# Kernel optimization log

Hardware: AMD Instinct MI355X
Metric: run time of the kernel (lower is better)

## Reference

```python
import jax, jax.numpy as jnp
import numpy as np

NUM_NODES = 50000
NUM_EDGES = 800000
NUM_GRAPHS = 1024
D_IN = 64
D_PROT = 1280
HID = 256
OUT = 1


def setup_inputs() -> dict:
    key = jax.random.key(0)
    ks = jax.random.split(key, 16)
    s = 0.02
    x = jax.random.normal(ks[0], (NUM_NODES, D_IN), dtype=jnp.float32)
    edge_index = jax.random.randint(ks[1], (2, NUM_EDGES), 0, NUM_NODES, dtype=jnp.int32)
    batch = jnp.sort(jax.random.randint(ks[2], (NUM_NODES,), 0, NUM_GRAPHS, dtype=jnp.int32))
    protein_embedding = jax.random.normal(ks[3], (NUM_GRAPHS, D_PROT), dtype=jnp.float32)
    # SAGEConv params: lin_l (aggregated neighbors, with bias), lin_r (self, no bias)
    Wl = jax.random.normal(ks[4], (D_IN, HID), dtype=jnp.float32) * s
    bl = jnp.zeros((HID,), dtype=jnp.float32)
    Wr = jax.random.normal(ks[5], (D_IN, HID), dtype=jnp.float32) * s
    Wp = jax.random.normal(ks[6], (D_PROT, HID), dtype=jnp.float32) * s
    bp = jnp.zeros((HID,), dtype=jnp.float32)
    Wi = jax.random.normal(ks[7], (2 * HID, HID), dtype=jnp.float32) * s
    bi = jnp.zeros((HID,), dtype=jnp.float32)
    Wo = jax.random.normal(ks[8], (HID, OUT), dtype=jnp.float32) * s
    bo = jnp.zeros((OUT,), dtype=jnp.float32)
    return {"x": x, "protein_embedding": protein_embedding, "Wl": Wl, "bl": bl,
            "Wr": Wr, "Wp": Wp, "bp": bp, "Wi": Wi, "bi": bi, "Wo": Wo, "bo": bo,
            "edge_index": edge_index, "batch": batch}


def _segment_mean(vals, seg_ids, num_segments):
    sums = jax.ops.segment_sum(vals, seg_ids, num_segments=num_segments)
    cnt = jax.ops.segment_sum(jnp.ones((vals.shape[0],), vals.dtype), seg_ids,
                              num_segments=num_segments)
    return sums / jnp.maximum(cnt, 1.0)[:, None]


def reference(x, protein_embedding, Wl, bl, Wr, Wp, bp, Wi, bi, Wo, bo, edge_index, batch):
    src, dst = edge_index[0], edge_index[1]
    # SAGEConv: mean-aggregate neighbor messages at target nodes, then fuse linears
    aggr = _segment_mean(x[src], dst, NUM_NODES)           # [N, D_IN]
    drug_x = jax.nn.relu(aggr @ Wl + bl + x @ Wr)          # [N, HID]
    # global_mean_pool over graphs in the batch
    pooled = _segment_mean(drug_x, batch, NUM_GRAPHS)      # [G, HID]
    protein_x = protein_embedding @ Wp + bp                # [G, HID]
    combined = jnp.concatenate((pooled, protein_x), axis=1)  # [G, 2*HID]
    interaction = jax.nn.relu(combined @ Wi + bi)          # [G, HID]
    return interaction @ Wo + bo                           # [G, OUT]
```

## Files before the change

### kernel.cpp

```cpp
#include <hip/hip_runtime.h>
#include <hip/hip_bf16.h>

#define N_NODES 50000
#define N_EDGES 800000
#define N_GRAPHS 1024
#define D_IN 64
#define D_PROT 1280
#define HID 256
#define N_PAD 50048

#define NB 782
#define BCAP 2048
#define BEPB 4096
#define BBLK 196

typedef __attribute__((ext_vector_type(8))) short short8;
typedef __attribute__((ext_vector_type(4))) float f32x4;
typedef __hip_bfloat16 bf16;

__device__ inline unsigned bf16rne(float f) {
  unsigned u = __float_as_uint(f);
  return (u + 0x7fffu + ((u >> 16) & 1u)) >> 16;
}
__device__ inline void acc_bf2(float4& a, uint2 v) {
  a.x += __uint_as_float(v.x << 16);
  a.y += __uint_as_float(v.x & 0xffff0000u);
  a.z += __uint_as_float(v.y << 16);
  a.w += __uint_as_float(v.y & 0xffff0000u);
}

#define PREP_XC 3125
#define PREP_PE (PREP_XC + 1280)
#define PREP_PL (PREP_PE + 8)
#define PREP_PR (PREP_PL + 8)
#define PREP_WP (PREP_PR + 160)
#define PREP_WI (PREP_WP + 64)

__device__ inline void pack_frag(const float* __restrict__ src, bf16* __restrict__ dst,
                                 int KC, int tid) {
  int lane = tid & 63;
  int chunk = tid >> 6;
  int c = chunk / KC, kc = chunk - c * KC;
  int kbase = kc * 32 + ((lane >> 4) * 8);
  int n = c * 16 + (lane & 15);
#pragma unroll
  for (int j = 0; j < 8; ++j)
    dst[(size_t)tid * 8 + j] = __float2bfloat16(src[(size_t)(kbase + j) * HID + n]);
}

__global__ __launch_bounds__(256) void k_front(
    const float* __restrict__ x, const float* __restrict__ pe,
    const float* __restrict__ Wl, const float* __restrict__ Wr,
    const float* __restrict__ Wp, const float* __restrict__ Wi,
    const int* __restrict__ ei,
    uint2* __restrict__ x2, uint2* __restrict__ pe2,
    bf16* __restrict__ Wl_pk, bf16* __restrict__ Wr_pk,
    bf16* __restrict__ Wp_pk, bf16* __restrict__ Wi_pk,
    int* __restrict__ bcnt, unsigned* __restrict__ bped) {
  __shared__ int hist[NB];
  __shared__ int base[NB];
  const int b = blockIdx.x;
  const int t = threadIdx.x;
  if (b < BBLK) {
    const int e0 = b * BEPB;
    for (int i = t; i < NB; i += 256) hist[i] = 0;
    __syncthreads();
    for (int i = t; i < BEPB; i += 1024) {
      int d[4]; bool v[4];
#pragma unroll
      for (int u = 0; u < 4; ++u) {
        int idx = i + u * 256;
        v[u] = (e0 + idx < N_EDGES);
        d[u] = v[u] ? ei[N_EDGES + e0 + idx] : 0;
      }
#pragma unroll
      for (int u = 0; u < 4; ++u)
        if (v[u]) atomicAdd(&hist[d[u] >> 6], 1);
    }
    __syncthreads();
    for (int i = t; i < NB; i += 256) {
      int c = hist[i];
      base[i] = (c > 0) ? atomicAdd(&bcnt[i], c) : 0;
      hist[i] = 0;
    }
    __syncthreads();
    for (int i = t; i < BEPB; i += 1024) {
      int s[4], d[4]; bool v[4];
#pragma unroll
      for (int u = 0; u < 4; ++u) {
        int idx = i + u * 256;
        v[u] = (e0 + idx < N_EDGES);
        s[u] = v[u] ? ei[e0 + idx] : 0;
        d[u] = v[u] ? ei[N_EDGES + e0 + idx] : 0;
      }
#pragma unroll
      for (int u = 0; u < 4; ++u) {
        if (v[u]) {
          int bk = d[u] >> 6;
          int pos = base[bk] + atomicAdd(&hist[bk], 1);
          if (pos < BCAP)
            bped[(size_t)bk * BCAP + pos] =
                (unsigned)s[u] | ((unsigned)(d[u] & 63) << 16);
        }
      }
    }
    return;
  }
  const int pb = b - BBLK;
  if (pb < PREP_XC) {
    int tid = pb * 256 + t;
    float4 v = ((const float4*)x)[tid];
    x2[tid] = make_uint2(bf16rne(v.x) | (bf16rne(v.y) << 16),
                         bf16rne(v.z) | (bf16rne(v.w) << 16));
  } else if (pb < PREP_PE) {
    int tid = (pb - PREP_XC) * 256 + t;
    float4 v = ((const float4*)pe)[tid];
    pe2[tid] = make_uint2(bf16rne(v.x) | (bf16rne(v.y) << 16),
                          bf16rne(v.z) | (bf16rne(v.w) << 16));
  } else if (pb < PREP_PL) {
    pack_frag(Wl, Wl_pk, 2, (pb - PREP_PE) * 256 + t);
  } else if (pb < PREP_PR) {
    pack_frag(Wr, Wr_pk, 2, (pb - PREP_PL) * 256 + t);
  } else if (pb < PREP_WP) {
    pack_frag(Wp, Wp_pk, 40, (pb - PREP_PR) * 256 + t);
  } else {
    pack_frag(Wi, Wi_pk, 16, (pb - PREP_WP) * 256 + t);
  }
}

__global__ __launch_bounds__(256) void k_mid(
    const uint2* __restrict__ x2, const unsigned* __restrict__ bped,
    const int* __restrict__ bcnt, uint2* __restrict__ a2,
    const bf16* __restrict__ pebf, const bf16* __restrict__ Wp_pk,
    float* __restrict__ prot4) {
  __shared__ unsigned s_raw[BCAP];
  __shared__ unsigned short s_e[BCAP];
  __shared__ int s_off[65];
  __shared__ int s_cur[64];
  const int t = threadIdx.x;
  if (blockIdx.x < NB) {
    const int b = blockIdx.x;
    const int nE = min(bcnt[b], BCAP);
    if (t < 64) s_cur[t] = 0;
    __syncthreads();
    for (int i = t; i < nE; i += 256) {
      unsigned pk = bped[(size_t)b * BCAP + i];
      s_raw[i] = pk;
      atomicAdd(&s_cur[(pk >> 16) & 63], 1);
    }
    __syncthreads();
    if (t < 64) {
      int sc = s_cur[t];
#pragma unroll
      for (int off = 1; off < 64; off <<= 1) {
        int u = __shfl_up(sc, off);
        if (t >= off) sc += u;
      }
      s_off[t + 1] = sc;
      if (t == 0) s_off[0] = 0;
      s_cur[t] = 0;
    }
    __syncthreads();
    for (int i = t; i < nE; i += 256) {
      unsigned pk = s_raw[i];
      int ld = (pk >> 16) & 63;
      int pos = s_off[ld] + atomicAdd(&s_cur[ld], 1);
      s_e[pos] = (unsigned short)(pk & 0xffffu);
    }
    __syncthreads();

    const int w = t >> 6, lane = t & 63;
    const int el = lane >> 4;
    const int fb = lane & 15;
    for (int n = w; n < 64; n += 4) {
      const int beg = s_off[n], end = s_off[n + 1];
      float4 s0 = {0,0,0,0}, s1 = {0,0,0,0}, s2 = {0,0,0,0}, s3 = {0,0,0,0};
      int e = beg;
      for (; e + 16 <= end; e += 16) {
        int i0 = s_e[e + el],     i1 = s_e[e + 4 + el];
        int i2 = s_e[e + 8 + el], i3 = s_e[e + 12 + el];
        uint2 v0 = x2[(size_t)i0 * 16 + fb];
        uint2 v1 = x2[(size_t)i1 * 16 + fb];
        uint2 v2 = x2[(size_t)i2 * 16 + fb];
        uint2 v3 = x2[(size_t)i3 * 16 + fb];
        acc_bf2(s0, v0); acc_bf2(s1, v1); acc_bf2(s2, v2); acc_bf2(s3, v3);
      }
      for (; e + 4 <= end; e += 4)
        acc_bf2(s0, x2[(size_t)s_e[e + el] * 16 + fb]);
      if (e + el < end)
        acc_bf2(s1, x2[(size_t)s_e[e + el] * 16 + fb]);
      float4 tt;
      tt.x = (s0.x + s1.x) + (s2.x + s3.x);
      tt.y = (s0.y + s1.y) + (s2.y + s3.y);
      tt.z = (s0.z + s1.z) + (s2.z + s3.z);
      tt.w = (s0.w + s1.w) + (s2.w + s3.w);
      tt.x += __shfl_xor(tt.x, 32); tt.x += __shfl_xor(tt.x, 16);
      tt.y += __shfl_xor(tt.y, 32); tt.y += __shfl_xor(tt.y, 16);
      tt.z += __shfl_xor(tt.z, 32); tt.z += __shfl_xor(tt.z, 16);
      tt.w += __shfl_xor(tt.w, 32); tt.w += __shfl_xor(tt.w, 16);
      const int node = b * 64 + n;
      if (el == 0 && node < N_NODES) {
        float inv = 1.0f / (float)max(end - beg, 1);
        uint2 o;
        o.x = bf16rne(tt.x * inv) | (bf16rne(tt.y * inv) << 16);
        o.y = bf16rne(tt.z * inv) | (bf16rne(tt.w * inv) << 16);
        a2[(size_t)node * 16 + fb] = o;
      }
    }
    return;
  }
  const int kb = blockIdx.x - NB;
  const int w = t >> 6, lane = t & 63;
  const int ml = lane & 15, q = lane >> 4;
  const int mt = kb >> 2, ks = kb & 3;
  const int g0 = mt * 16, kc0 = ks * 10;
  f32x4 acc[4];
#pragma unroll
  for (int c = 0; c < 4; ++c) acc[c] = (f32x4){0.f, 0.f, 0.f, 0.f};
  for (int kc = kc0; kc < kc0 + 10; ++kc) {
    short8 a = *(const short8*)(pebf + (size_t)(g0 + ml) * D_PROT + kc * 32 + q * 8);
#pragma unroll
    for (int cl = 0; cl < 4; ++cl) {
      short8 bb = *(const short8*)(Wp_pk + ((size_t)((w * 4 + cl) * 40 + kc) * 64 + lane) * 8);
      acc[cl] = __builtin_amdgcn_mfma_f32_16x16x32_bf16(a, bb, acc[cl], 0, 0, 0);
    }
  }
#pragma unroll
  for (int cl = 0; cl < 4; ++cl) {
    const int col = w * 64 + cl * 16 + ml;
#pragma unroll
    for (int i = 0; i < 4; ++i)
      prot4[((size_t)ks * N_GRAPHS + g0 + q * 4 + i) * HID + col] = acc[cl][i];
  }
}

__global__ __launch_bounds__(256) void k_mlp(
    const bf16* __restrict__ aggrbf, const bf16* __restrict__ xbf,
    const bf16* __restrict__ Wl_pk, const bf16* __restrict__ Wr_pk,
    const float* __restrict__ bl, unsigned short* __restrict__ drug) {
  const int t = threadIdx.x, w = t >> 6, lane = t & 63;
  const int ml = lane & 15, q = lane >> 4;
  const int n0 = blockIdx.x * 64;

  f32x4 acc[4][4];
#pragma unroll
  for (int a = 0; a < 4; ++a)
#pragma unroll
    for (int c = 0; c < 4; ++c) acc[a][c] = (f32x4){0.f, 0.f, 0.f, 0.f};

#pragma unroll
  for (int mat = 0; mat < 2; ++mat) {
    const bf16* A = mat ? xbf : aggrbf;
    const bf16* B = mat ? Wr_pk : Wl_pk;
#pragma unroll
    for (int kc = 0; kc < 2; ++kc) {
      short8 af[4], bfr[4];
#pragma unroll
      for (int rt = 0; rt < 4; ++rt)
        af[rt] = *(const short8*)(A + (size_t)(n0 + rt * 16 + ml) * D_IN + kc * 32 + q * 8);
#pragma unroll
      for (int cl = 0; cl < 4; ++cl)
        bfr[cl] = *(const short8*)(B + ((size_t)((w * 4 + cl) * 2 + kc) * 64 + lane) * 8);
#pragma unroll
      for (int rt = 0; rt < 4; ++rt)
#pragma unroll
        for (int cl = 0; cl < 4; ++cl)
          acc[rt][cl] = __builtin_amdgcn_mfma_f32_16x16x32_bf16(af[rt], bfr[cl], acc[rt][cl], 0, 0, 0);
    }
  }

#pragma unroll
  for (int cl = 0; cl < 4; ++cl) {
    const int col = w * 64 + cl * 16 + ml;
    const float bias = bl[col];
#pragma unroll
    for (int rt = 0; rt < 4; ++rt) {
#pragma unroll
      for (int i = 0; i < 4; ++i) {
        const int row = n0 + rt * 16 + q * 4 + i;
        drug[(size_t)row * HID + col] =
            (unsigned short)bf16rne(fmaxf(acc[rt][cl][i] + bias, 0.f));
      }
    }
  }
}

__device__ inline int lb_dev(const int* __restrict__ a, int v) {
  int lo = 0, hi = N_NODES;
  while (lo < hi) { int m = (lo + hi) >> 1; if (a[m] < v) lo = m + 1; else hi = m; }
  return lo;
}

__global__ __launch_bounds__(256) void k_pool(
    const unsigned short* __restrict__ drug, const int* __restrict__ batch,
    const float* __restrict__ prot4, const float* __restrict__ bp,
    unsigned short* __restrict__ comb) {
  const int t = threadIdx.x;
  if (blockIdx.x < N_GRAPHS) {
    const int g = blockIdx.x;
    const int lo = lb_dev(batch, g);
    const int hi = lb_dev(batch, g + 1);
    float s0 = 0.f, s1 = 0.f, s2 = 0.f, s3 = 0.f;
    float s4 = 0.f, s5 = 0.f, s6 = 0.f, s7 = 0.f;
    int r = lo;
    for (; r + 8 <= hi; r += 8) {
      s0 += __uint_as_float((unsigned)drug[(size_t)(r + 0) * HID + t] << 16);
      s1 += __uint_as_float((unsigned)drug[(size_t)(r + 1) * HID + t] << 16);
      s2 += __uint_as_float((unsigned)drug[(size_t)(r + 2) * HID + t] << 16);
      s3 += __uint_as_float((unsigned)drug[(size_t)(r + 3) * HID + t] << 16);
      s4 += __uint_as_float((unsigned)drug[(size_t)(r + 4) * HID + t] << 16);
      s5 += __uint_as_float((unsigned)drug[(size_t)(r + 5) * HID + t] << 16);
      s6 += __uint_as_float((unsigned)drug[(size_t)(r + 6) * HID + t] << 16);
      s7 += __uint_as_float((unsigned)drug[(size_t)(r + 7) * HID + t] << 16);
    }
    for (; r < hi; ++r)
      s0 += __uint_as_float((unsigned)drug[(size_t)r * HID + t] << 16);
    float inv = 1.0f / (float)max(hi - lo, 1);
    float m = (((s0 + s1) + (s2 + s3)) + ((s4 + s5) + (s6 + s7))) * inv;
    comb[(size_t)g * 512 + t] = (unsigned short)bf16rne(m);
    return;
  }
  const int pb = blockIdx.x - N_GRAPHS;
#pragma unroll
  for (int g = 0; g < 4; ++g) {
    const int gg = pb * 4 + g;
    size_t idx = (size_t)gg * HID + t;
    float pr = prot4[idx] + prot4[(size_t)N_GRAPHS * HID + idx]
             + prot4[2 * (size_t)N_GRAPHS * HID + idx]
             + prot4[3 * (size_t)N_GRAPHS * HID + idx];
    comb[(size_t)gg * 512 + HID + t] = (unsigned short)bf16rne(pr + bp[t]);
  }
}

__global__ __launch_bounds__(256) void k_tail(
    const bf16* __restrict__ comb, const bf16* __restrict__ Wi_pk,
    const float* __restrict__ bi, const float* __restrict__ Wo,
    const float* __restrict__ bo, float* __restrict__ out) {
  __shared__ float sRed[16 * 4];
  const int t = threadIdx.x, w = t >> 6, lane = t & 63;
  const int ml = lane & 15, q = lane >> 4;
  const int g0 = blockIdx.x * 16;
  f32x4 acc[4];
#pragma unroll
  for (int c = 0; c < 4; ++c) acc[c] = (f32x4){0.f, 0.f, 0.f, 0.f};
  for (int kc = 0; kc < 16; ++kc) {
    short8 a = *(const short8*)(comb + (size_t)(g0 + ml) * 512 + kc * 32 + q * 8);
#pragma unroll
    for (int cl = 0; cl < 4; ++cl) {
      short8 bb = *(const short8*)(Wi_pk + ((size_t)((w * 4 + cl) * 16 + kc) * 64 + lane) * 8);
      acc[cl] = __builtin_amdgcn_mfma_f32_16x16x32_bf16(a, bb, acc[cl], 0, 0, 0);
    }
  }
  float bic[4], woc[4];
#pragma unroll
  for (int cl = 0; cl < 4; ++cl) {
    const int col = w * 64 + cl * 16 + ml;
    bic[cl] = bi[col];
    woc[cl] = Wo[col];
  }
#pragma unroll
  for (int i = 0; i < 4; ++i) {
    float s = 0.f;
#pragma unroll
    for (int cl = 0; cl < 4; ++cl)
      s += fmaxf(acc[cl][i] + bic[cl], 0.f) * woc[cl];
    s += __shfl_xor(s, 1); s += __shfl_xor(s, 2);
    s += __shfl_xor(s, 4); s += __shfl_xor(s, 8);
    if (ml == 0) sRed[(q * 4 + i) * 4 + w] = s;
  }
  __syncthreads();
  if (t < 16)
    out[g0 + t] = sRed[t * 4 + 0] + sRed[t * 4 + 1] + sRed[t * 4 + 2]
                + sRed[t * 4 + 3] + bo[0];
}

extern "C" void kernel_launch(void* const* d_in, const int* in_sizes, int n_in,
                              void* d_out, int out_size, void* d_ws, size_t ws_size,
                              hipStream_t stream) {
  const float* x     = (const float*)d_in[0];
  const float* pe    = (const float*)d_in[1];
  const float* Wl    = (const float*)d_in[2];
  const float* bl    = (const float*)d_in[3];
  const float* Wr    = (const float*)d_in[4];
  const float* Wp    = (const float*)d_in[5];
  const float* bp    = (const float*)d_in[6];
  const float* Wi    = (const float*)d_in[7];
  const float* bi    = (const float*)d_in[8];
  const float* Wo    = (const float*)d_in[9];
  const float* bo    = (const float*)d_in[10];
  const int*   ei    = (const int*)d_in[11];
  const int*   batch = (const int*)d_in[12];
  float* out = (float*)d_out;

  char* p = (char*)d_ws;
  auto alloc = [&](size_t bytes) {
    char* r = p;
    p += (bytes + 255) & ~(size_t)255;
    return r;
  };
  int*      bcnt  = (int*)alloc(NB * 4);
  size_t zbytes = (size_t)(p - (char*)d_ws);
  unsigned* bped  = (unsigned*)alloc((size_t)NB * BCAP * 4);
  bf16*  xbf    = (bf16*)alloc((size_t)N_PAD * D_IN * 2);
  bf16*  aggrbf = (bf16*)alloc((size_t)N_PAD * D_IN * 2);
  bf16*  pebf   = (bf16*)alloc((size_t)N_GRAPHS * D_PROT * 2);
  bf16*  Wl_pk  = (bf16*)alloc((size_t)D_IN * HID * 2);
  bf16*  Wr_pk  = (bf16*)alloc((size_t)D_IN * HID * 2);
  bf16*  Wp_pk  = (bf16*)alloc((size_t)D_PROT * HID * 2);
  bf16*  Wi_pk  = (bf16*)alloc((size_t)2 * HID * HID * 2);
  float* prot4  = (float*)alloc((size_t)4 * N_GRAPHS * HID * 4);
  unsigned short* drug = (unsigned short*)alloc((size_t)N_PAD * HID * 2);
  unsigned short* comb = (unsigned short*)alloc((size_t)N_GRAPHS * 2 * HID * 2);

  (void)hipMemsetAsync(d_ws, 0, zbytes, stream);

  k_front<<<BBLK + PREP_WI, 256, 0, stream>>>(
      x, pe, Wl, Wr, Wp, Wi, ei,
      (uint2*)xbf, (uint2*)pebf, Wl_pk, Wr_pk, Wp_pk, Wi_pk, bcnt, bped);
  k_mid<<<NB + 256, 256, 0, stream>>>(
      (const uint2*)xbf, bped, bcnt, (uint2*)aggrbf, pebf, Wp_pk, prot4);
  k_mlp<<<N_PAD / 64, 256, 0, stream>>>(aggrbf, xbf, Wl_pk, Wr_pk, bl, drug);
  k_pool<<<N_GRAPHS + 256, 256, 0, stream>>>(drug, batch, prot4, bp, comb);
  k_tail<<<N_GRAPHS / 16, 256, 0, stream>>>((const bf16*)comb, Wi_pk, bi, Wo, bo, out);
}
```

Baseline: 171.1 us.

## Fuse neighbor aggregation with SAGE linear layers and drop split-K protein GEMM

Merges the mean-aggregation kernel and the node MLP kernel so each block keeps its 64 aggregated rows in shared memory and immediately runs the Wl/Wr MFMA GEMM. This removes the aggregated-feature round trip through global memory and one kernel launch. The protein projection now runs as a full-K GEMM in 64 blocks and writes bf16 with bias straight into the combined buffer, which drops the fp32 split-K partials and their reduction in the pool kernel. The trade-off is more shared memory and registers per block in the fused kernel, and fewer, longer protein blocks.

```diff
diff --git a/kernel.cpp b/kernel.cpp
--- a/kernel.cpp
+++ b/kernel.cpp
@@ -13,6 +13,8 @@
 #define BCAP 2048
 #define BEPB 4096
 #define BBLK 196
+
+#define AGG_STRIDE 72
 
 typedef __attribute__((ext_vector_type(8))) short short8;
 typedef __attribute__((ext_vector_type(4))) float f32x4;
@@ -128,16 +130,22 @@
   }
 }
 
-__global__ __launch_bounds__(256) void k_mid(
+__global__ __launch_bounds__(256) void k_fuse(
     const uint2* __restrict__ x2, const unsigned* __restrict__ bped,
-    const int* __restrict__ bcnt, uint2* __restrict__ a2,
+    const int* __restrict__ bcnt, const bf16* __restrict__ xbf,
+    const bf16* __restrict__ Wl_pk, const bf16* __restrict__ Wr_pk,
+    const float* __restrict__ bl,
     const bf16* __restrict__ pebf, const bf16* __restrict__ Wp_pk,
-    float* __restrict__ prot4) {
+    const float* __restrict__ bp,
+    unsigned short* __restrict__ drug, unsigned short* __restrict__ comb) {
   __shared__ unsigned s_raw[BCAP];
   __shared__ unsigned short s_e[BCAP];
   __shared__ int s_off[65];
   __shared__ int s_cur[64];
+  __shared__ unsigned short s_agg[64 * AGG_STRIDE];
   const int t = threadIdx.x;
+  const int w = t >> 6, lane = t & 63;
+  const int ml = lane & 15, q = lane >> 4;
   if (blockIdx.x < NB) {
     const int b = blockIdx.x;
     const int nE = min(bcnt[b], BCAP);
@@ -169,9 +177,8 @@
     }
     __syncthreads();
 
-    const int w = t >> 6, lane = t & 63;
-    const int el = lane >> 4;
-    const int fb = lane & 15;
+    const int el = q;
+    const int fb = ml;
     for (int n = w; n < 64; n += 4) {
       const int beg = s_off[n], end = s_off[n + 1];
       float4 s0 = {0,0,0,0}, s1 = {0,0,0,0}, s2 = {0,0,0,0}, s3 = {0,0,0,0};
@@ -198,26 +205,73 @@
       tt.y += __shfl_xor(tt.y, 32); tt.y += __shfl_xor(tt.y, 16);
       tt.z += __shfl_xor(tt.z, 32); tt.z += __shfl_xor(tt.z, 16);
       tt.w += __shfl_xor(tt.w, 32); tt.w += __shfl_xor(tt.w, 16);
-      const int node = b * 64 + n;
-      if (el == 0 && node < N_NODES) {
+      if (el == 0) {
         float inv = 1.0f / (float)max(end - beg, 1);
         uint2 o;
         o.x = bf16rne(tt.x * inv) | (bf16rne(tt.y * inv) << 16);
         o.y = bf16rne(tt.z * inv) | (bf16rne(tt.w * inv) << 16);
-        a2[(size_t)node * 16 + fb] = o;
+        *(uint2*)(s_agg + n * AGG_STRIDE + fb * 4) = o;
+      }
+    }
+    __syncthreads();
+
+    const int n0 = b * 64;
+    f32x4 acc[4][4];
+#pragma unroll
+    for (int a = 0; a < 4; ++a)
+#pragma unroll
+      for (int c = 0; c < 4; ++c) acc[a][c] = (f32x4){0.f, 0.f, 0.f, 0.f};
+#pragma unroll
+    for (int kc = 0; kc < 2; ++kc) {
+      short8 af[4], bfr[4];
+#pragma unroll
+      for (int rt = 0; rt < 4; ++rt)
+        af[rt] = *(const short8*)(s_agg + (rt * 16 + ml) * AGG_STRIDE + kc * 32 + q * 8);
+#pragma unroll
+      for (int cl = 0; cl < 4; ++cl)
+        bfr[cl] = *(const short8*)(Wl_pk + ((size_t)((w * 4 + cl) * 2 + kc) * 64 + lane) * 8);
+#pragma unroll
+      for (int rt = 0; rt < 4; ++rt)
+#pragma unroll
+        for (int cl = 0; cl < 4; ++cl)
+          acc[rt][cl] = __builtin_amdgcn_mfma_f32_16x16x32_bf16(af[rt], bfr[cl], acc[rt][cl], 0, 0, 0);
+    }
+#pragma unroll
+    for (int kc = 0; kc < 2; ++kc) {
+      short8 af[4], bfr[4];
+#pragma unroll
+      for (int rt = 0; rt < 4; ++rt)
+        af[rt] = *(const short8*)(xbf + (size_t)(n0 + rt * 16 + ml) * D_IN + kc * 32 + q * 8);
+#pragma unroll
+      for (int cl = 0; cl < 4; ++cl)
+        bfr[cl] = *(const short8*)(Wr_pk + ((size_t)((w * 4 + cl) * 2 + kc) * 64 + lane) * 8);
+#pragma unroll
+      for (int rt = 0; rt < 4; ++rt)
+#pragma unroll
+        for (int cl = 0; cl < 4; ++cl)
+          acc[rt][cl] = __builtin_amdgcn_mfma_f32_16x16x32_bf16(af[rt], bfr[cl], acc[rt][cl], 0, 0, 0);
+    }
+#pragma unroll
+    for (int cl = 0; cl < 4; ++cl) {
+      const int col = w * 64 + cl * 16 + ml;
+      const float bias = bl[col];
+#pragma unroll
+      for (int rt = 0; rt < 4; ++rt) {
+#pragma unroll
+        for (int i = 0; i < 4; ++i) {
+          const int row = n0 + rt * 16 + q * 4 + i;
+          drug[(size_t)row * HID + col] =
+              (unsigned short)bf16rne(fmaxf(acc[rt][cl][i] + bias, 0.f));
+        }
       }
     }
     return;
   }
-  const int kb = blockIdx.x - NB;
-  const int w = t >> 6, lane = t & 63;
-  const int ml = lane & 15, q = lane >> 4;
-  const int mt = kb >> 2, ks = kb & 3;
-  const int g0 = mt * 16, kc0 = ks * 10;
+  const int g0 = (blockIdx.x - NB) * 16;
   f32x4 acc[4];
 #pragma unroll
   for (int c = 0; c < 4; ++c) acc[c] = (f32x4){0.f, 0.f, 0.f, 0.f};
-  for (int kc = kc0; kc < kc0 + 10; ++kc) {
+  for (int kc = 0; kc < 40; ++kc) {
     short8 a = *(const short8*)(pebf + (size_t)(g0 + ml) * D_PROT + kc * 32 + q * 8);
 #pragma unroll
     for (int cl = 0; cl < 4; ++cl) {
@@ -228,60 +282,11 @@
 #pragma unroll
   for (int cl = 0; cl < 4; ++cl) {
     const int col = w * 64 + cl * 16 + ml;
+    const float bias = bp[col];
 #pragma unroll
     for (int i = 0; i < 4; ++i)
-      prot4[((size_t)ks * N_GRAPHS + g0 + q * 4 + i) * HID + col] = acc[cl][i];
-  }
-}
-
-__global__ __launch_bounds__(256) void k_mlp(
-    const bf16* __restrict__ aggrbf, const bf16* __restrict__ xbf,
-    const bf16* __restrict__ Wl_pk, const bf16* __restrict__ Wr_pk,
-    const float* __restrict__ bl, unsigned short* __restrict__ drug) {
-  const int t = threadIdx.x, w = t >> 6, lane = t & 63;
-  const int ml = lane & 15, q = lane >> 4;
-  const int n0 = blockIdx.x * 64;
-
-  f32x4 acc[4][4];
-#pragma unroll
-  for (int a = 0; a < 4; ++a)
-#pragma unroll
-    for (int c = 0; c < 4; ++c) acc[a][c] = (f32x4){0.f, 0.f, 0.f, 0.f};
-
-#pragma unroll
-  for (int mat = 0; mat < 2; ++mat) {
-    const bf16* A = mat ? xbf : aggrbf;
-    const bf16* B = mat ? Wr_pk : Wl_pk;
-#pragma unroll
-    for (int kc = 0; kc < 2; ++kc) {
-      short8 af[4], bfr[4];
-#pragma unroll
-      for (int rt = 0; rt < 4; ++rt)
-        af[rt] = *(const short8*)(A + (size_t)(n0 + rt * 16 + ml) * D_IN + kc * 32 + q * 8);
-#pragma unroll
-      for (int cl = 0; cl < 4; ++cl)
-        bfr[cl] = *(const short8*)(B + ((size_t)((w * 4 + cl) * 2 + kc) * 64 + lane) * 8);
-#pragma unroll
-      for (int rt = 0; rt < 4; ++rt)
-#pragma unroll
-        for (int cl = 0; cl < 4; ++cl)
-          acc[rt][cl] = __builtin_amdgcn_mfma_f32_16x16x32_bf16(af[rt], bfr[cl], acc[rt][cl], 0, 0, 0);
-    }
-  }
-
-#pragma unroll
-  for (int cl = 0; cl < 4; ++cl) {
-    const int col = w * 64 + cl * 16 + ml;
-    const float bias = bl[col];
-#pragma unroll
-    for (int rt = 0; rt < 4; ++rt) {
-#pragma unroll
-      for (int i = 0; i < 4; ++i) {
-        const int row = n0 + rt * 16 + q * 4 + i;
-        drug[(size_t)row * HID + col] =
-            (unsigned short)bf16rne(fmaxf(acc[rt][cl][i] + bias, 0.f));
-      }
-    }
+      comb[(size_t)(g0 + q * 4 + i) * 512 + HID + col] =
+          (unsigned short)bf16rne(acc[cl][i] + bias);
   }
 }
 
@@ -293,43 +298,28 @@
 
 __global__ __launch_bounds__(256) void k_pool(
     const unsigned short* __restrict__ drug, const int* __restrict__ batch,
-    const float* __restrict__ prot4, const float* __restrict__ bp,
     unsigned short* __restrict__ comb) {
-  const int t = threadIdx.x;
-  if (blockIdx.x < N_GRAPHS) {
-    const int g = blockIdx.x;
-    const int lo = lb_dev(batch, g);
-    const int hi = lb_dev(batch, g + 1);
-    float s0 = 0.f, s1 = 0.f, s2 = 0.f, s3 = 0.f;
-    float s4 = 0.f, s5 = 0.f, s6 = 0.f, s7 = 0.f;
-    int r = lo;
-    for (; r + 8 <= hi; r += 8) {
-      s0 += __uint_as_float((unsigned)drug[(size_t)(r + 0) * HID + t] << 16);
-      s1 += __uint_as_float((unsigned)drug[(size_t)(r + 1) * HID + t] << 16);
-      s2 += __uint_as_float((unsigned)drug[(size_t)(r + 2) * HID + t] << 16);
-      s3 += __uint_as_float((unsigned)drug[(size_t)(r + 3) * HID + t] << 16);
-      s4 += __uint_as_float((unsigned)drug[(size_t)(r + 4) * HID + t] << 16);
-      s5 += __uint_as_float((unsigned)drug[(size_t)(r + 5) * HID + t] << 16);
-      s6 += __uint_as_float((unsigned)drug[(size_t)(r + 6) * HID + t] << 16);
-      s7 += __uint_as_float((unsigned)drug[(size_t)(r + 7) * HID + t] << 16);
-    }
-    for (; r < hi; ++r)
-      s0 += __uint_as_float((unsigned)drug[(size_t)r * HID + t] << 16);
-    float inv = 1.0f / (float)max(hi - lo, 1);
-    float m = (((s0 + s1) + (s2 + s3)) + ((s4 + s5) + (s6 + s7))) * inv;
-    comb[(size_t)g * 512 + t] = (unsigned short)bf16rne(m);
-    return;
-  }
-  const int pb = blockIdx.x - N_GRAPHS;
-#pragma unroll
-  for (int g = 0; g < 4; ++g) {
-    const int gg = pb * 4 + g;
-    size_t idx = (size_t)gg * HID + t;
-    float pr = prot4[idx] + prot4[(size_t)N_GRAPHS * HID + idx]
-             + prot4[2 * (size_t)N_GRAPHS * HID + idx]
-             + prot4[3 * (size_t)N_GRAPHS * HID + idx];
-    comb[(size_t)gg * 512 + HID + t] = (unsigned short)bf16rne(pr + bp[t]);
-  }
+  const int g = blockIdx.x, t = threadIdx.x;
+  const int lo = lb_dev(batch, g);
+  const int hi = lb_dev(batch, g + 1);
+  float s0 = 0.f, s1 = 0.f, s2 = 0.f, s3 = 0.f;
+  float s4 = 0.f, s5 = 0.f, s6 = 0.f, s7 = 0.f;
+  int r = lo;
+  for (; r + 8 <= hi; r += 8) {
+    s0 += __uint_as_float((unsigned)drug[(size_t)(r + 0) * HID + t] << 16);
+    s1 += __uint_as_float((unsigned)drug[(size_t)(r + 1) * HID + t] << 16);
+    s2 += __uint_as_float((unsigned)drug[(size_t)(r + 2) * HID + t] << 16);
+    s3 += __uint_as_float((unsigned)drug[(size_t)(r + 3) * HID + t] << 16);
+    s4 += __uint_as_float((unsigned)drug[(size_t)(r + 4) * HID + t] << 16);
+    s5 += __uint_as_float((unsigned)drug[(size_t)(r + 5) * HID + t] << 16);
+    s6 += __uint_as_float((unsigned)drug[(size_t)(r + 6) * HID + t] << 16);
+    s7 += __uint_as_float((unsigned)drug[(size_t)(r + 7) * HID + t] << 16);
+  }
+  for (; r < hi; ++r)
+    s0 += __uint_as_float((unsigned)drug[(size_t)r * HID + t] << 16);
+  float inv = 1.0f / (float)max(hi - lo, 1);
+  float m = (((s0 + s1) + (s2 + s3)) + ((s4 + s5) + (s6 + s7))) * inv;
+  comb[(size_t)g * 512 + t] = (unsigned short)bf16rne(m);
 }
 
 __global__ __launch_bounds__(256) void k_tail(
@@ -402,13 +392,11 @@
   size_t zbytes = (size_t)(p - (char*)d_ws);
   unsigned* bped  = (unsigned*)alloc((size_t)NB * BCAP * 4);
   bf16*  xbf    = (bf16*)alloc((size_t)N_PAD * D_IN * 2);
-  bf16*  aggrbf = (bf16*)alloc((size_t)N_PAD * D_IN * 2);
   bf16*  pebf   = (bf16*)alloc((size_t)N_GRAPHS * D_PROT * 2);
   bf16*  Wl_pk  = (bf16*)alloc((size_t)D_IN * HID * 2);
   bf16*  Wr_pk  = (bf16*)alloc((size_t)D_IN * HID * 2);
   bf16*  Wp_pk  = (bf16*)alloc((size_t)D_PROT * HID * 2);
   bf16*  Wi_pk  = (bf16*)alloc((size_t)2 * HID * HID * 2);
-  float* prot4  = (float*)alloc((size_t)4 * N_GRAPHS * HID * 4);
   unsigned short* drug = (unsigned short*)alloc((size_t)N_PAD * HID * 2);
   unsigned short* comb = (unsigned short*)alloc((size_t)N_GRAPHS * 2 * HID * 2);
 
@@ -417,9 +405,9 @@
   k_front<<<BBLK + PREP_WI, 256, 0, stream>>>(
       x, pe, Wl, Wr, Wp, Wi, ei,
       (uint2*)xbf, (uint2*)pebf, Wl_pk, Wr_pk, Wp_pk, Wi_pk, bcnt, bped);
-  k_mid<<<NB + 256, 256, 0, stream>>>(
-      (const uint2*)xbf, bped, bcnt, (uint2*)aggrbf, pebf, Wp_pk, prot4);
-  k_mlp<<<N_PAD / 64, 256, 0, stream>>>(aggrbf, xbf, Wl_pk, Wr_pk, bl, drug);
-  k_pool<<<N_GRAPHS + 256, 256, 0, stream>>>(drug, batch, prot4, bp, comb);
+  k_fuse<<<NB + 64, 256, 0, stream>>>(
+      (const uint2*)xbf, bped, bcnt, xbf, Wl_pk, Wr_pk, bl,
+      pebf, Wp_pk, bp, drug, comb);
+  k_pool<<<N_GRAPHS, 256, 0, stream>>>(drug, batch, comb);
   k_tail<<<N_GRAPHS / 16, 256, 0, stream>>>((const bf16*)comb, Wi_pk, bi, Wo, bo, out);
 }
```

Measured after the change: 185.7 us. 1.09x slower.

## Precompute graph boundaries, drop split-K protein GEMM, and cache dst in registers

Applied to the files above, without the earlier changes.

Graph start offsets are now built from the sorted batch array in the front kernel, which removes the per-block binary searches in the pool kernel. The protein GEMM no longer splits K four ways into a partial-sum buffer. Each of 64 blocks runs the full K loop and writes bias-added bf16 straight into the combined buffer, which drops the prot4 round trip and its reduction blocks but leaves less parallelism for that GEMM. The bucketing pass keeps the destination indices in registers between the histogram and scatter phases, and the mid kernel re-reads bucket entries from global memory instead of staging them in shared memory.

```diff
diff --git a/kernel.cpp b/kernel.cpp
--- a/kernel.cpp
+++ b/kernel.cpp
@@ -35,6 +35,7 @@
 #define PREP_PR (PREP_PL + 8)
 #define PREP_WP (PREP_PR + 160)
 #define PREP_WI (PREP_WP + 64)
+#define PREP_GB (PREP_WI + 196)
 
 __device__ inline void pack_frag(const float* __restrict__ src, bf16* __restrict__ dst,
                                  int KC, int tid) {
@@ -52,11 +53,12 @@
     const float* __restrict__ x, const float* __restrict__ pe,
     const float* __restrict__ Wl, const float* __restrict__ Wr,
     const float* __restrict__ Wp, const float* __restrict__ Wi,
-    const int* __restrict__ ei,
+    const int* __restrict__ ei, const int* __restrict__ batch,
     uint2* __restrict__ x2, uint2* __restrict__ pe2,
     bf16* __restrict__ Wl_pk, bf16* __restrict__ Wr_pk,
     bf16* __restrict__ Wp_pk, bf16* __restrict__ Wi_pk,
-    int* __restrict__ bcnt, unsigned* __restrict__ bped) {
+    int* __restrict__ bcnt, unsigned* __restrict__ bped,
+    int* __restrict__ gb) {
   __shared__ int hist[NB];
   __shared__ int base[NB];
   const int b = blockIdx.x;
@@ -65,18 +67,17 @@
     const int e0 = b * BEPB;
     for (int i = t; i < NB; i += 256) hist[i] = 0;
     __syncthreads();
-    for (int i = t; i < BEPB; i += 1024) {
-      int d[4]; bool v[4];
+    int dc[16];
+#pragma unroll
+    for (int o = 0; o < 4; ++o)
 #pragma unroll
       for (int u = 0; u < 4; ++u) {
-        int idx = i + u * 256;
-        v[u] = (e0 + idx < N_EDGES);
-        d[u] = v[u] ? ei[N_EDGES + e0 + idx] : 0;
-      }
-#pragma unroll
-      for (int u = 0; u < 4; ++u)
-        if (v[u]) atomicAdd(&hist[d[u] >> 6], 1);
-    }
+        int e = e0 + o * 1024 + u * 256 + t;
+        dc[o * 4 + u] = (e < N_EDGES) ? ei[N_EDGES + e] : -1;
+      }
+#pragma unroll
+    for (int j = 0; j < 16; ++j)
+      if (dc[j] >= 0) atomicAdd(&hist[dc[j] >> 6], 1);
     __syncthreads();
     for (int i = t; i < NB; i += 256) {
       int c = hist[i];
@@ -84,23 +85,23 @@
       hist[i] = 0;
     }
     __syncthreads();
-    for (int i = t; i < BEPB; i += 1024) {
-      int s[4], d[4]; bool v[4];
+#pragma unroll
+    for (int o = 0; o < 4; ++o) {
+      int sc[4];
 #pragma unroll
       for (int u = 0; u < 4; ++u) {
-        int idx = i + u * 256;
-        v[u] = (e0 + idx < N_EDGES);
-        s[u] = v[u] ? ei[e0 + idx] : 0;
-        d[u] = v[u] ? ei[N_EDGES + e0 + idx] : 0;
+        int e = e0 + o * 1024 + u * 256 + t;
+        sc[u] = (e < N_EDGES) ? ei[e] : 0;
       }
 #pragma unroll
       for (int u = 0; u < 4; ++u) {
-        if (v[u]) {
-          int bk = d[u] >> 6;
+        int d = dc[o * 4 + u];
+        if (d >= 0) {
+          int bk = d >> 6;
           int pos = base[bk] + atomicAdd(&hist[bk], 1);
           if (pos < BCAP)
             bped[(size_t)bk * BCAP + pos] =
-                (unsigned)s[u] | ((unsigned)(d[u] & 63) << 16);
+                (unsigned)sc[u] | ((unsigned)(d & 63) << 16);
         }
       }
     }
@@ -123,8 +124,17 @@
     pack_frag(Wr, Wr_pk, 2, (pb - PREP_PL) * 256 + t);
   } else if (pb < PREP_WP) {
     pack_frag(Wp, Wp_pk, 40, (pb - PREP_PR) * 256 + t);
+  } else if (pb < PREP_WI) {
+    pack_frag(Wi, Wi_pk, 16, (pb - PREP_WP) * 256 + t);
   } else {
-    pack_frag(Wi, Wi_pk, 16, (pb - PREP_WP) * 256 + t);
+    int n = (pb - PREP_WI) * 256 + t;
+    if (n < N_NODES) {
+      int bc = batch[n];
+      int bprev = (n == 0) ? -1 : batch[n - 1];
+      for (int g = bprev + 1; g <= bc; ++g) gb[g] = n;
+      if (n == N_NODES - 1)
+        for (int g = bc + 1; g <= N_GRAPHS; ++g) gb[g] = N_NODES;
+    }
   }
 }
 
@@ -132,22 +142,21 @@
     const uint2* __restrict__ x2, const unsigned* __restrict__ bped,
     const int* __restrict__ bcnt, uint2* __restrict__ a2,
     const bf16* __restrict__ pebf, const bf16* __restrict__ Wp_pk,
-    float* __restrict__ prot4) {
-  __shared__ unsigned s_raw[BCAP];
+    const float* __restrict__ bp, unsigned short* __restrict__ comb) {
   __shared__ unsigned short s_e[BCAP];
   __shared__ int s_off[65];
   __shared__ int s_cur[64];
   const int t = threadIdx.x;
+  const int w = t >> 6, lane = t & 63;
+  const int ml = lane & 15, q = lane >> 4;
   if (blockIdx.x < NB) {
     const int b = blockIdx.x;
     const int nE = min(bcnt[b], BCAP);
+    const unsigned* bpp = bped + (size_t)b * BCAP;
     if (t < 64) s_cur[t] = 0;
     __syncthreads();
-    for (int i = t; i < nE; i += 256) {
-      unsigned pk = bped[(size_t)b * BCAP + i];
-      s_raw[i] = pk;
-      atomicAdd(&s_cur[(pk >> 16) & 63], 1);
-    }
+    for (int i = t; i < nE; i += 256)
+      atomicAdd(&s_cur[(bpp[i] >> 16) & 63], 1);
     __syncthreads();
     if (t < 64) {
       int sc = s_cur[t];
@@ -162,16 +171,15 @@
     }
     __syncthreads();
     for (int i = t; i < nE; i += 256) {
-      unsigned pk = s_raw[i];
+      unsigned pk = bpp[i];
       int ld = (pk >> 16) & 63;
       int pos = s_off[ld] + atomicAdd(&s_cur[ld], 1);
       s_e[pos] = (unsigned short)(pk & 0xffffu);
     }
     __syncthreads();
 
-    const int w = t >> 6, lane = t & 63;
-    const int el = lane >> 4;
-    const int fb = lane & 15;
+    const int el = q & 3;
+    const int fb = ml;
     for (int n = w; n < 64; n += 4) {
       const int beg = s_off[n], end = s_off[n + 1];
       float4 s0 = {0,0,0,0}, s1 = {0,0,0,0}, s2 = {0,0,0,0}, s3 = {0,0,0,0};
@@ -209,15 +217,11 @@
     }
     return;
   }
-  const int kb = blockIdx.x - NB;
-  const int w = t >> 6, lane = t & 63;
-  const int ml = lane & 15, q = lane >> 4;
-  const int mt = kb >> 2, ks = kb & 3;
-  const int g0 = mt * 16, kc0 = ks * 10;
+  const int g0 = (blockIdx.x - NB) * 16;
   f32x4 acc[4];
 #pragma unroll
   for (int c = 0; c < 4; ++c) acc[c] = (f32x4){0.f, 0.f, 0.f, 0.f};
-  for (int kc = kc0; kc < kc0 + 10; ++kc) {
+  for (int kc = 0; kc < 40; ++kc) {
     short8 a = *(const short8*)(pebf + (size_t)(g0 + ml) * D_PROT + kc * 32 + q * 8);
 #pragma unroll
     for (int cl = 0; cl < 4; ++cl) {
@@ -228,9 +232,11 @@
 #pragma unroll
   for (int cl = 0; cl < 4; ++cl) {
     const int col = w * 64 + cl * 16 + ml;
+    const float bias = bp[col];
 #pragma unroll
     for (int i = 0; i < 4; ++i)
-      prot4[((size_t)ks * N_GRAPHS + g0 + q * 4 + i) * HID + col] = acc[cl][i];
+      comb[(size_t)(g0 + q * 4 + i) * 512 + HID + col] =
+          (unsigned short)bf16rne(acc[cl][i] + bias);
   }
 }
 
@@ -285,51 +291,29 @@
   }
 }
 
-__device__ inline int lb_dev(const int* __restrict__ a, int v) {
-  int lo = 0, hi = N_NODES;
-  while (lo < hi) { int m = (lo + hi) >> 1; if (a[m] < v) lo = m + 1; else hi = m; }
-  return lo;
-}
-
 __global__ __launch_bounds__(256) void k_pool(
-    const unsigned short* __restrict__ drug, const int* __restrict__ batch,
-    const float* __restrict__ prot4, const float* __restrict__ bp,
+    const unsigned short* __restrict__ drug, const int* __restrict__ gb,
     unsigned short* __restrict__ comb) {
-  const int t = threadIdx.x;
-  if (blockIdx.x < N_GRAPHS) {
-    const int g = blockIdx.x;
-    const int lo = lb_dev(batch, g);
-    const int hi = lb_dev(batch, g + 1);
-    float s0 = 0.f, s1 = 0.f, s2 = 0.f, s3 = 0.f;
-    float s4 = 0.f, s5 = 0.f, s6 = 0.f, s7 = 0.f;
-    int r = lo;
-    for (; r + 8 <= hi; r += 8) {
-      s0 += __uint_as_float((unsigned)drug[(size_t)(r + 0) * HID + t] << 16);
-      s1 += __uint_as_float((unsigned)drug[(size_t)(r + 1) * HID + t] << 16);
-      s2 += __uint_as_float((unsigned)drug[(size_t)(r + 2) * HID + t] << 16);
-      s3 += __uint_as_float((unsigned)drug[(size_t)(r + 3) * HID + t] << 16);
-      s4 += __uint_as_float((unsigned)drug[(size_t)(r + 4) * HID + t] << 16);
-      s5 += __uint_as_float((unsigned)drug[(size_t)(r + 5) * HID + t] << 16);
-      s6 += __uint_as_float((unsigned)drug[(size_t)(r + 6) * HID + t] << 16);
-      s7 += __uint_as_float((unsigned)drug[(size_t)(r + 7) * HID + t] << 16);
-    }
-    for (; r < hi; ++r)
-      s0 += __uint_as_float((unsigned)drug[(size_t)r * HID + t] << 16);
-    float inv = 1.0f / (float)max(hi - lo, 1);
-    float m = (((s0 + s1) + (s2 + s3)) + ((s4 + s5) + (s6 + s7))) * inv;
-    comb[(size_t)g * 512 + t] = (unsigned short)bf16rne(m);
-    return;
-  }
-  const int pb = blockIdx.x - N_GRAPHS;
-#pragma unroll
-  for (int g = 0; g < 4; ++g) {
-    const int gg = pb * 4 + g;
-    size_t idx = (size_t)gg * HID + t;
-    float pr = prot4[idx] + prot4[(size_t)N_GRAPHS * HID + idx]
-             + prot4[2 * (size_t)N_GRAPHS * HID + idx]
-             + prot4[3 * (size_t)N_GRAPHS * HID + idx];
-    comb[(size_t)gg * 512 + HID + t] = (unsigned short)bf16rne(pr + bp[t]);
-  }
+  const int g = blockIdx.x, t = threadIdx.x;
+  const int lo = gb[g], hi = gb[g + 1];
+  float s0 = 0.f, s1 = 0.f, s2 = 0.f, s3 = 0.f;
+  float s4 = 0.f, s5 = 0.f, s6 = 0.f, s7 = 0.f;
+  int r = lo;
+  for (; r + 8 <= hi; r += 8) {
+    s0 += __uint_as_float((unsigned)drug[(size_t)(r + 0) * HID + t] << 16);
+    s1 += __uint_as_float((unsigned)drug[(size_t)(r + 1) * HID + t] << 16);
+    s2 += __uint_as_float((unsigned)drug[(size_t)(r + 2) * HID + t] << 16);
+    s3 += __uint_as_float((unsigned)drug[(size_t)(r + 3) * HID + t] << 16);
+    s4 += __uint_as_float((unsigned)drug[(size_t)(r + 4) * HID + t] << 16);
+    s5 += __uint_as_float((unsigned)drug[(size_t)(r + 5) * HID + t] << 16);
+    s6 += __uint_as_float((unsigned)drug[(size_t)(r + 6) * HID + t] << 16);
+    s7 += __uint_as_float((unsigned)drug[(size_t)(r + 7) * HID + t] << 16);
+  }
+  for (; r < hi; ++r)
+    s0 += __uint_as_float((unsigned)drug[(size_t)r * HID + t] << 16);
+  float inv = 1.0f / (float)max(hi - lo, 1);
+  float m = (((s0 + s1) + (s2 + s3)) + ((s4 + s5) + (s6 + s7))) * inv;
+  comb[(size_t)g * 512 + t] = (unsigned short)bf16rne(m);
 }
 
 __global__ __launch_bounds__(256) void k_tail(
@@ -408,18 +392,19 @@
   bf16*  Wr_pk  = (bf16*)alloc((size_t)D_IN * HID * 2);
   bf16*  Wp_pk  = (bf16*)alloc((size_t)D_PROT * HID * 2);
   bf16*  Wi_pk  = (bf16*)alloc((size_t)2 * HID * HID * 2);
-  float* prot4  = (float*)alloc((size_t)4 * N_GRAPHS * HID * 4);
+  int*   gb     = (int*)alloc((N_GRAPHS + 1) * 4);
   unsigned short* drug = (unsigned short*)alloc((size_t)N_PAD * HID * 2);
   unsigned short* comb = (unsigned short*)alloc((size_t)N_GRAPHS * 2 * HID * 2);
 
   (void)hipMemsetAsync(d_ws, 0, zbytes, stream);
 
-  k_front<<<BBLK + PREP_WI, 256, 0, stream>>>(
-      x, pe, Wl, Wr, Wp, Wi, ei,
-      (uint2*)xbf, (uint2*)pebf, Wl_pk, Wr_pk, Wp_pk, Wi_pk, bcnt, bped);
-  k_mid<<<NB + 256, 256, 0, stream>>>(
-      (const uint2*)xbf, bped, bcnt, (uint2*)aggrbf, pebf, Wp_pk, prot4);
+  k_front<<<BBLK + PREP_GB, 256, 0, stream>>>(
+      x, pe, Wl, Wr, Wp, Wi, ei, batch,
+      (uint2*)xbf, (uint2*)pebf, Wl_pk, Wr_pk, Wp_pk, Wi_pk, bcnt, bped, gb);
+  k_mid<<<NB + 64, 256, 0, stream>>>(
+      (const uint2*)xbf, bped, bcnt, (uint2*)aggrbf, pebf, Wp_pk, bp,
+      comb);
   k_mlp<<<N_PAD / 64, 256, 0, stream>>>(aggrbf, xbf, Wl_pk, Wr_pk, bl, drug);
-  k_pool<<<N_GRAPHS + 256, 256, 0, stream>>>(drug, batch, prot4, bp, comb);
+  k_pool<<<N_GRAPHS, 256, 0, stream>>>(drug, gb, comb);
   k_tail<<<N_GRAPHS / 16, 256, 0, stream>>>((const bf16*)comb, Wi_pk, bi, Wo, bo, out);
 }
```

After: 182.0 us. 1.06x slower.
